# Kernel tuning notes

Hardware: AMD Instinct MI355X
Metric: run time of the kernel (lower is better)

Reference implementation:

```python
import math
import jax, jax.numpy as jnp
import numpy as np

FACTOR = 1  # self.factor
B, L, H, E = 16, 2048, 8, 64


def setup_inputs() -> dict:
    key = jax.random.key(0)
    kq, kk, kv = jax.random.split(key, 3)
    queries = jax.random.normal(kq, (B, L, H, E), dtype=jnp.float32)
    keys = jax.random.normal(kk, (B, L, H, E), dtype=jnp.float32)
    values = jax.random.normal(kv, (B, L, H, E), dtype=jnp.float32)
    return {"queries": queries, "keys": keys, "values": values}


def reference(queries, keys, values):
    # AutoCorrelation forward, agg_mode='speed', inference path (train=False),
    # norm=False, Q == K == V lengths so the pad/truncate branch is a no-op.
    Bb, Ll, Hh, Ee = queries.shape
    # Permute to [B, H, E, L] as the torch code does before FFT / aggregation.
    qp = jnp.transpose(queries, (0, 2, 3, 1))
    kp = jnp.transpose(keys, (0, 2, 3, 1))
    vp = jnp.transpose(values, (0, 2, 3, 1))
    # (1) period-based dependency discovery: circular cross-correlation via FFT
    q_fft = jnp.fft.rfft(qp, axis=-1)
    k_fft = jnp.fft.rfft(kp, axis=-1)
    corr = jnp.fft.irfft(q_fft * jnp.conj(k_fft), n=Ll, axis=-1)  # [B,H,E,L]
    # (2) time delay aggregation (speed mode, inference):
    k = int(FACTOR * math.log(Ll))
    mean_r_qk = jnp.mean(corr, axis=(1, 2))  # mean over head then channel -> [B,L]
    r_qk_top, tao = jax.lax.top_k(mean_r_qk, k)  # [B,k]
    weights = jax.nn.softmax(r_qk_top, axis=-1)  # [B,k]
    # gather into values repeated twice along L  <=>  circular roll by tao
    idx = (jnp.arange(Ll)[None, None, :] + tao[:, :, None]) % Ll  # [B,k,L]
    # [B,1,H,E,L] gathered with [B,k,1,1,L] -> [B,k,H,E,L]
    gathered = jnp.take_along_axis(vp[:, None], idx[:, :, None, None, :], axis=-1)
    agg = jnp.einsum('bk,bkhel->bhel', weights, gathered)  # softmax-weighted sum
    # back to [B, L, H, E]
    return jnp.transpose(agg, (0, 3, 1, 2))
```

## Files before the change

kernel.cpp:

```cpp
#include <hip/hip_runtime.h>
#include <math.h>

#define LN      2048
#define LOG2L   11
#define BB      16
#define HE      512
#define KTOP    7
#define TWO_PI  6.283185307179586f
#define RC      0.70710678118654752f

#define SIG(e)  ((e) ^ (((e) >> 5) & 31))

struct c32 { float x, y; };
__device__ __forceinline__ c32 cmul(c32 a, c32 b) {
    return { a.x * b.x - a.y * b.y, a.x * b.y + a.y * b.x };
}
__device__ __forceinline__ c32 cadd(c32 a, c32 b) { return { a.x + b.x, a.y + b.y }; }
__device__ __forceinline__ c32 csub(c32 a, c32 b) { return { a.x - b.x, a.y - b.y }; }

__device__ __forceinline__ void dft4(c32 a, c32 b, c32 c, c32 d,
                                     c32& y0, c32& y1, c32& y2, c32& y3) {
    c32 t0 = cadd(a, c), t1 = csub(a, c);
    c32 t2 = cadd(b, d);
    c32 t3 = { b.y - d.y, d.x - b.x };
    y0 = cadd(t0, t2);
    y1 = cadd(t1, t3);
    y2 = csub(t0, t2);
    y3 = csub(t1, t3);
}

__device__ __forceinline__ void dft8(const c32* x, c32* y) {
    c32 e0, e1, e2, e3, o0, o1, o2, o3;
    dft4(x[0], x[2], x[4], x[6], e0, e1, e2, e3);
    dft4(x[1], x[3], x[5], x[7], o0, o1, o2, o3);
    c32 p1 = { RC * (o1.x + o1.y), RC * (o1.y - o1.x) };
    c32 p2 = { o2.y, -o2.x };
    c32 p3 = { RC * (o3.y - o3.x), -RC * (o3.x + o3.y) };
    y[0] = cadd(e0, o0); y[4] = csub(e0, o0);
    y[1] = cadd(e1, p1); y[5] = csub(e1, p1);
    y[2] = cadd(e2, p2); y[6] = csub(e2, p2);
    y[3] = cadd(e3, p3); y[7] = csub(e3, p3);
}

__device__ __forceinline__ void mk_tw(int pm, c32* W) {
    float sn, cs;
    __sincosf(-(TWO_PI / (float)LN) * (float)pm, &sn, &cs);
    const c32 w1 = { cs, sn };
    const c32 w2 = cmul(w1, w1);
    const c32 w3 = cmul(w1, w2);
    const c32 w4 = cmul(w2, w2);
    W[0] = w1; W[1] = w2; W[2] = w3; W[3] = w4;
    W[4] = cmul(w1, w4); W[5] = cmul(w2, w4); W[6] = cmul(w3, w4);
}

template<int LOG2M>
__device__ __forceinline__ void r8_ld(float2* Z, int tid, const c32* TW) {
    c32 v[8];
    #pragma unroll
    for (int r = 0; r < 8; ++r) {
        float2 z = Z[SIG(tid + (r << 8))];
        v[r] = { z.x, z.y };
    }
    c32 y[8];
    dft8(v, y);
    #pragma unroll
    for (int kk = 1; kk < 8; ++kk) y[kk] = cmul(y[kk], TW[kk - 1]);
    __syncthreads();
    const int q_ = tid & ((1 << LOG2M) - 1);
    const int ob = q_ + ((tid - q_) << 3);
    #pragma unroll
    for (int kk = 0; kk < 8; ++kk)
        Z[SIG(ob + (kk << LOG2M))] = make_float2(y[kk].x, y[kk].y);
    __syncthreads();
}

__device__ __forceinline__ void r4_final_wg(float2* Z, int tid) {
    c32 v[2][4];
    #pragma unroll
    for (int u = 0; u < 2; ++u) {
        const int j = tid + (u << 8);
        #pragma unroll
        for (int r = 0; r < 4; ++r) {
            float2 z = Z[SIG(j + (r << 9))];
            v[u][r] = { z.x, z.y };
        }
    }
    __syncthreads();
    #pragma unroll
    for (int u = 0; u < 2; ++u) {
        const int j = tid + (u << 8);
        c32 y0, y1, y2, y3;
        dft4(v[u][0], v[u][1], v[u][2], v[u][3], y0, y1, y2, y3);
        Z[SIG(j)]        = make_float2(y0.x, y0.y);
        Z[SIG(j + 512)]  = make_float2(y1.x, y1.y);
        Z[SIG(j + 1024)] = make_float2(y2.x, y2.y);
        Z[SIG(j + 1536)] = make_float2(y3.x, y3.y);
    }
    __syncthreads();
}

__global__ __launch_bounds__(256) void transpose_pack_kernel(
    const float* __restrict__ q, const float* __restrict__ k,
    float* __restrict__ qT, float* __restrict__ kT) {
    __shared__ float2 tile[64][65];
    const int tid = threadIdx.x;
    const int bid = blockIdx.x;
    const int b  = bid >> 8;
    const int lt = (bid >> 3) & 31;
    const int ct = bid & 7;
    const int l0 = lt << 6, c0 = ct << 6;
    const int g16 = tid >> 4;
    const int m16 = (tid & 15) << 2;
    #pragma unroll
    for (int ii = 0; ii < 4; ++ii) {
        const int r = g16 + (ii << 4);
        const size_t src = ((size_t)(b * LN + l0 + r)) * HE + c0 + m16;
        const float4 qv = *(const float4*)(q + src);
        const float4 kv = *(const float4*)(k + src);
        tile[r][m16 + 0] = make_float2(qv.x, kv.x);
        tile[r][m16 + 1] = make_float2(qv.y, kv.y);
        tile[r][m16 + 2] = make_float2(qv.z, kv.z);
        tile[r][m16 + 3] = make_float2(qv.w, kv.w);
    }
    __syncthreads();
    #pragma unroll
    for (int ii = 0; ii < 4; ++ii) {
        const int rc = g16 + (ii << 4);
        const float2 t0 = tile[m16 + 0][rc];
        const float2 t1 = tile[m16 + 1][rc];
        const float2 t2 = tile[m16 + 2][rc];
        const float2 t3 = tile[m16 + 3][rc];
        const size_t dst = ((size_t)(b * HE + c0 + rc)) * LN + l0 + m16;
        *(float4*)(qT + dst) = make_float4(t0.x, t1.x, t2.x, t3.x);
        *(float4*)(kT + dst) = make_float4(t0.y, t1.y, t2.y, t3.y);
    }
}

__global__ __launch_bounds__(256) void fft_reg0_kernel(
    const float* __restrict__ qT, const float* __restrict__ kT,
    float* __restrict__ spec ) {
    __shared__ float2 Z[LN];
    const int tid = threadIdx.x;
    const int wg  = blockIdx.x;
    const int b   = wg >> 7;
    const int c0  = (wg & 127) << 2;

    c32 TW0[7], TW1[7], TW2[7];
    mk_tw(tid, TW0);
    mk_tw(tid & ~7, TW1);
    mk_tw(tid & ~63, TW2);

    float accx[4], accy[4];
    #pragma unroll
    for (int i = 0; i < 4; ++i) { accx[i] = 0.f; accy[i] = 0.f; }
    float a1024 = 0.f;

    const size_t base0 = ((size_t)(b * HE + c0)) << LOG2L;
    c32 v[8];
    #pragma unroll
    for (int r = 0; r < 8; ++r) {
        v[r].x = qT[base0 + tid + (r << 8)];
        v[r].y = kT[base0 + tid + (r << 8)];
    }

    #pragma unroll 1
    for (int ch = 0; ch < 4; ++ch) {
        c32 y[8];
        dft8(v, y);
        #pragma unroll
        for (int kk = 1; kk < 8; ++kk) y[kk] = cmul(y[kk], TW0[kk - 1]);
        __syncthreads();
        #pragma unroll
        for (int kk = 0; kk < 8; ++kk)
            Z[SIG((tid << 3) + kk)] = make_float2(y[kk].x, y[kk].y);
        __syncthreads();

        if (ch < 3) {
            const size_t basen = base0 + ((size_t)(ch + 1) << LOG2L);
            #pragma unroll
            for (int r = 0; r < 8; ++r) {
                v[r].x = qT[basen + tid + (r << 8)];
                v[r].y = kT[basen + tid + (r << 8)];
            }
        }

        r8_ld<3>(Z, tid, TW1);
        r8_ld<6>(Z, tid, TW2);
        r4_final_wg(Z, tid);

        #pragma unroll
        for (int i = 0; i < 4; ++i) {
            const int f = tid + (i << 8);
            const int g = (LN - f) & (LN - 1);
            const float2 zf = Z[SIG(f)];
            const float2 zm = Z[SIG(g)];
            const float Qr = 0.5f * (zf.x + zm.x);
            const float Qi = 0.5f * (zf.y - zm.y);
            const float Kr = 0.5f * (zf.y + zm.y);
            const float Ki = -0.5f * (zf.x - zm.x);
            accx[i] += Qr * Kr + Qi * Ki;
            accy[i] += Qi * Kr - Qr * Ki;
        }
        if (tid == 0) {
            const float2 zf = Z[SIG(1024)];
            a1024 += zf.x * zf.y;
        }
    }
    #pragma unroll
    for (int i = 0; i < 4; ++i) {
        const int f = tid + (i << 8);
        atomicAdd(&spec[((size_t)b * LN + f) * 2 + 0], accx[i]);
        atomicAdd(&spec[((size_t)b * LN + f) * 2 + 1], accy[i]);
    }
    if (tid == 0)
        atomicAdd(&spec[((size_t)b * LN + 1024) * 2 + 0], a1024);
}

template<int LOG2M>
__device__ __forceinline__ void r8_stage(float2* Z, int lane) {
    c32 v[32];
    #pragma unroll
    for (int u = 0; u < 4; ++u) {
        const int j = lane + (u << 6);
        #pragma unroll
        for (int r = 0; r < 8; ++r) {
            float2 z = Z[SIG(j + (r << 8))];
            v[(u << 3) + r] = { z.x, z.y };
        }
    }
    c32 y[32];
    #pragma unroll
    for (int u = 0; u < 4; ++u) {
        const int j  = lane + (u << 6);
        const int pm = j & ~((1 << LOG2M) - 1);
        dft8(&v[u << 3], &y[u << 3]);
        float sn, cs;
        __sincosf(-(TWO_PI / (float)LN) * (float)pm, &sn, &cs);
        c32 base = { cs, sn };
        c32 t = base;
        #pragma unroll
        for (int kk = 1; kk < 8; ++kk) {
            y[(u << 3) + kk] = cmul(y[(u << 3) + kk], t);
            if (kk < 7) t = cmul(t, base);
        }
    }
    __syncthreads();
    #pragma unroll
    for (int u = 0; u < 4; ++u) {
        const int j  = lane + (u << 6);
        const int q_ = j & ((1 << LOG2M) - 1);
        const int ob = q_ + ((j - q_) << 3);
        #pragma unroll
        for (int kk = 0; kk < 8; ++kk) {
            c32 yy = y[(u << 3) + kk];
            Z[SIG(ob + (kk << LOG2M))] = make_float2(yy.x, yy.y);
        }
    }
    __syncthreads();
}

__device__ __forceinline__ void r4_final(float2* Z, int lane) {
    c32 v[32];
    #pragma unroll
    for (int u = 0; u < 8; ++u) {
        const int j = lane + (u << 6);
        #pragma unroll
        for (int r = 0; r < 4; ++r) {
            float2 z = Z[SIG(j + (r << 9))];
            v[(u << 2) + r] = { z.x, z.y };
        }
    }
    __syncthreads();
    #pragma unroll
    for (int u = 0; u < 8; ++u) {
        const int j = lane + (u << 6);
        c32 y0, y1, y2, y3;
        dft4(v[u << 2], v[(u << 2) + 1], v[(u << 2) + 2], v[(u << 2) + 3],
             y0, y1, y2, y3);
        Z[SIG(j)]        = make_float2(y0.x, y0.y);
        Z[SIG(j + 512)]  = make_float2(y1.x, y1.y);
        Z[SIG(j + 1024)] = make_float2(y2.x, y2.y);
        Z[SIG(j + 1536)] = make_float2(y3.x, y3.y);
    }
    __syncthreads();
}

__global__ __launch_bounds__(256) void fft_fused_kernel(
    const float* __restrict__ qg, const float* __restrict__ kg,
    float* __restrict__ spec) {
    __shared__ float2 zb[4][LN];
    const int t    = threadIdx.x;
    const int bid  = blockIdx.x;
    const int wgid = ((bid & 7) << 8) | (bid >> 3);
    const int b    = wgid >> 7;
    const int c0   = (wgid & 127) << 2;
    #pragma unroll
    for (int i = 0; i < 8; ++i) {
        const int l = t + (i << 8);
        const size_t base = (size_t)(b * LN + l) * HE + c0;
        const float4 qv = *(const float4*)(qg + base);
        const float4 kv = *(const float4*)(kg + base);
        const int sl = SIG(l);
        zb[0][sl] = make_float2(qv.x, kv.x);
        zb[1][sl] = make_float2(qv.y, kv.y);
        zb[2][sl] = make_float2(qv.z, kv.z);
        zb[3][sl] = make_float2(qv.w, kv.w);
    }
    __syncthreads();
    const int w    = t >> 6;
    const int lane = t & 63;
    float2* Z = zb[w];
    r8_stage<0>(Z, lane);
    r8_stage<3>(Z, lane);
    r8_stage<6>(Z, lane);
    r4_final(Z, lane);
    float sx[32], sy[32];
    #pragma unroll
    for (int i = 0; i < 32; ++i) {
        const int f = lane + (i << 6);
        const float2 zf = Z[SIG(f)];
        const float2 zm = Z[SIG((LN - f) & (LN - 1))];
        const float Qr = 0.5f * (zf.x + zm.x);
        const float Qi = 0.5f * (zf.y - zm.y);
        const float Kr = 0.5f * (zf.y + zm.y);
        const float Ki = -0.5f * (zf.x - zm.x);
        sx[i] = Qr * Kr + Qi * Ki;
        sy[i] = Qi * Kr - Qr * Ki;
    }
    __syncthreads();
    #pragma unroll
    for (int i = 0; i < 32; ++i) {
        const int f = lane + (i << 6);
        Z[SIG(f)] = make_float2(sx[i], sy[i]);
    }
    __syncthreads();
    #pragma unroll
    for (int i = 0; i < 8; ++i) {
        const int f  = t + (i << 8);
        if (f <= 1024) {
            const int sf = SIG(f);
            const float rx = zb[0][sf].x + zb[1][sf].x + zb[2][sf].x + zb[3][sf].x;
            const float ry = zb[0][sf].y + zb[1][sf].y + zb[2][sf].y + zb[3][sf].y;
            atomicAdd(&spec[((size_t)b * LN + f) * 2 + 0], rx);
            atomicAdd(&spec[((size_t)b * LN + f) * 2 + 1], ry);
        }
    }
}

__device__ __forceinline__ unsigned bitrev11(unsigned x) {
    return __brev(x) >> (32 - LOG2L);
}

__global__ __launch_bounds__(256) void icorr_topk_kernel(
    const float* __restrict__ spec, float* __restrict__ wts, int* __restrict__ tao) {
    __shared__ float2 zbuf[LN];
    __shared__ float2 tw[LN / 2];
    __shared__ float  cr[LN];
    __shared__ float  rv[256];
    __shared__ int    ri[256];
    __shared__ float  topv[KTOP];
    __shared__ int    topi[KTOP];
    const int tid = threadIdx.x;
    const int b   = blockIdx.x;
    for (int p = tid; p < LN / 2; p += 256) {
        float s, c;
        sincosf(-TWO_PI * (float)p / (float)LN, &s, &c);
        tw[p] = make_float2(c, s);
    }
    for (int f = tid; f < LN; f += 256) {
        const int  fs  = (f <= 1024) ? f : (LN - f);
        const float sg = (f <= 1024) ? -1.f : 1.f;
        float sr = spec[((size_t)b * LN + fs) * 2 + 0];
        float si = spec[((size_t)b * LN + fs) * 2 + 1];
        zbuf[bitrev11((unsigned)f)] = make_float2(sr, sg * si);
    }
    __syncthreads();
    for (int s = 0; s < LOG2L; ++s) {
        const int half = 1 << s;
        for (int j = tid; j < LN / 2; j += 256) {
            const int grp = j >> s;
            const int pos = j & (half - 1);
            const int i0  = (grp << (s + 1)) + pos;
            const int i1  = i0 + half;
            const float2 w = tw[pos << (LOG2L - 1 - s)];
            float2 a  = zbuf[i0];
            float2 bv = zbuf[i1];
            float tr = w.x * bv.x - w.y * bv.y;
            float ti = w.x * bv.y + w.y * bv.x;
            zbuf[i0] = make_float2(a.x + tr, a.y + ti);
            zbuf[i1] = make_float2(a.x - tr, a.y - ti);
        }
        __syncthreads();
    }
    const float scale = 1.0f / ((float)LN * (float)HE);
    for (int t = tid; t < LN; t += 256) cr[t] = zbuf[t].x * scale;
    __syncthreads();
    for (int it = 0; it < KTOP; ++it) {
        float mv = -INFINITY;
        int   mi = 0;
        for (int t = tid; t < LN; t += 256) {
            float v = cr[t];
            if (v > mv) { mv = v; mi = t; }
        }
        rv[tid] = mv; ri[tid] = mi;
        __syncthreads();
        for (int off = 128; off > 0; off >>= 1) {
            if (tid < off) {
                float ov = rv[tid + off]; int oi = ri[tid + off];
                if (ov > rv[tid] || (ov == rv[tid] && oi < ri[tid])) {
                    rv[tid] = ov; ri[tid] = oi;
                }
            }
            __syncthreads();
        }
        if (tid == 0) {
            topv[it] = rv[0];
            topi[it] = ri[0];
            cr[ri[0]] = -INFINITY;
        }
        __syncthreads();
    }
    if (tid == 0) {
        float m = topv[0];
        float s = 0.f;
        float ex[KTOP];
        for (int j = 0; j < KTOP; ++j) { ex[j] = __expf(topv[j] - m); s += ex[j]; }
        float inv = 1.0f / s;
        for (int j = 0; j < KTOP; ++j) {
            wts[b * 8 + j] = ex[j] * inv;
            tao[b * 8 + j] = topi[j];
        }
    }
}

__global__ __launch_bounds__(256) void gather_kernel(
    const float* __restrict__ v, const float* __restrict__ wts,
    const int* __restrict__ tao, float* __restrict__ out) {
    __shared__ float lw[KTOP];
    __shared__ int   lt[KTOP];
    const int tid = threadIdx.x;
    const int bid = blockIdx.x;
    const int wg  = ((bid & 7) << 11) | (bid >> 3);
    const long long idx = (long long)wg * 256 + tid;
    const int c4 = (int)(idx & 127);
    const int l  = (int)((idx >> 7) & (LN - 1));
    const int b  = (int)(idx >> 18);
    if (tid < KTOP) {
        lw[tid] = wts[b * 8 + tid];
        lt[tid] = tao[b * 8 + tid];
    }
    __syncthreads();
    const float4* v4 = (const float4*)v;
    float4 a = make_float4(0.f, 0.f, 0.f, 0.f);
    #pragma unroll
    for (int j = 0; j < KTOP; ++j) {
        int ls = (l + lt[j]) & (LN - 1);
        float4 x = v4[((size_t)b * LN + ls) * 128 + c4];
        float w = lw[j];
        a.x += w * x.x; a.y += w * x.y; a.z += w * x.z; a.w += w * x.w;
    }
    ((float4*)out)[idx] = a;
}

extern "C" void kernel_launch(void* const* d_in, const int* in_sizes, int n_in,
                              void* d_out, int out_size, void* d_ws, size_t ws_size,
                              hipStream_t stream) {
    const float* q = (const float*)d_in[0];
    const float* k = (const float*)d_in[1];
    const float* v = (const float*)d_in[2];
    float* out = (float*)d_out;

    const size_t nT   = (size_t)BB * HE * LN;
    const size_t need = nT * 4 + (size_t)BB * LN * 2 * 4 + (size_t)BB * 8 * 8;

    if (ws_size >= need) {
        float* kT   = (float*)d_ws;
        float* spec = kT + nT;
        float* wts  = spec + (size_t)BB * LN * 2;
        int*   tao  = (int*)(wts + BB * 8);
        float* qT   = out;

        hipMemsetAsync(spec, 0, (size_t)BB * LN * 2 * sizeof(float), stream);
        transpose_pack_kernel<<<BB * 32 * 8, 256, 0, stream>>>(q, k, qT, kT);
        fft_reg0_kernel<<<BB * (HE / 4), 256, 0, stream>>>(qT, kT, spec);
        icorr_topk_kernel<<<BB, 256, 0, stream>>>(spec, wts, tao);
        const int n4 = BB * LN * HE / 4;
        gather_kernel<<<n4 / 256, 256, 0, stream>>>(v, wts, tao, out);
    } else {
        float* spec = (float*)d_ws;
        float* wts  = spec + (size_t)BB * LN * 2;
        int*   tao  = (int*)(wts + BB * 8);
        hipMemsetAsync(spec, 0, (size_t)BB * LN * 2 * sizeof(float), stream);
        fft_fused_kernel<<<BB * (HE / 4), 256, 0, stream>>>(q, k, spec);
        icorr_topk_kernel<<<BB, 256, 0, stream>>>(spec, wts, tao);
        const int n4 = BB * LN * HE / 4;
        gather_kernel<<<n4 / 256, 256, 0, stream>>>(v, wts, tao, out);
    }
}
```

Measured before the change: 173.4 us.

## Trim FFT kernel register use: recompute twiddles, drop prefetch, halve channels per block

The FFT kernel no longer keeps three precomputed twiddle arrays and a prefetched next-channel register buffer alive across the loop. Twiddles are recomputed with sincos inside each radix-8 stage, and each block now handles 2 channels instead of 4, which doubles the grid. Launch bounds request 8 blocks per CU. The aim is lower VGPR pressure and higher occupancy. The cost is extra sincos work, the loss of load/compute overlap within a block, and twice as many atomic or partial spectrum accumulations.

```diff
diff --git a/kernel.cpp b/kernel.cpp
--- a/kernel.cpp
+++ b/kernel.cpp
@@ -54,7 +54,7 @@
 }
 
 template<int LOG2M>
-__device__ __forceinline__ void r8_ld(float2* Z, int tid, const c32* TW) {
+__device__ __forceinline__ void r8_ld_t(float2* Z, int tid) {
     c32 v[8];
     #pragma unroll
     for (int r = 0; r < 8; ++r) {
@@ -63,8 +63,10 @@
     }
     c32 y[8];
     dft8(v, y);
-    #pragma unroll
-    for (int kk = 1; kk < 8; ++kk) y[kk] = cmul(y[kk], TW[kk - 1]);
+    c32 W[7];
+    mk_tw(tid & ~((1 << LOG2M) - 1), W);
+    #pragma unroll
+    for (int kk = 1; kk < 8; ++kk) y[kk] = cmul(y[kk], W[kk - 1]);
     __syncthreads();
     const int q_ = tid & ((1 << LOG2M) - 1);
     const int ob = q_ + ((tid - q_) << 3);
@@ -136,19 +138,14 @@
     }
 }
 
-__global__ __launch_bounds__(256) void fft_reg0_kernel(
+__global__ __launch_bounds__(256, 8) void fft_lean_kernel(
     const float* __restrict__ qT, const float* __restrict__ kT,
     float* __restrict__ spec ) {
     __shared__ float2 Z[LN];
     const int tid = threadIdx.x;
     const int wg  = blockIdx.x;
-    const int b   = wg >> 7;
-    const int c0  = (wg & 127) << 2;
-
-    c32 TW0[7], TW1[7], TW2[7];
-    mk_tw(tid, TW0);
-    mk_tw(tid & ~7, TW1);
-    mk_tw(tid & ~63, TW2);
+    const int b   = wg >> 8;
+    const int c0  = (wg & 255) << 1;
 
     float accx[4], accy[4];
     #pragma unroll
@@ -156,36 +153,32 @@
     float a1024 = 0.f;
 
     const size_t base0 = ((size_t)(b * HE + c0)) << LOG2L;
-    c32 v[8];
-    #pragma unroll
-    for (int r = 0; r < 8; ++r) {
-        v[r].x = qT[base0 + tid + (r << 8)];
-        v[r].y = kT[base0 + tid + (r << 8)];
-    }
 
     #pragma unroll 1
-    for (int ch = 0; ch < 4; ++ch) {
+    for (int ch = 0; ch < 2; ++ch) {
+        const size_t base = base0 + ((size_t)ch << LOG2L);
+        c32 v[8];
+        #pragma unroll
+        for (int r = 0; r < 8; ++r) {
+            v[r].x = qT[base + tid + (r << 8)];
+            v[r].y = kT[base + tid + (r << 8)];
+        }
         c32 y[8];
         dft8(v, y);
-        #pragma unroll
-        for (int kk = 1; kk < 8; ++kk) y[kk] = cmul(y[kk], TW0[kk - 1]);
+        {
+            c32 W[7];
+            mk_tw(tid, W);
+            #pragma unroll
+            for (int kk = 1; kk < 8; ++kk) y[kk] = cmul(y[kk], W[kk - 1]);
+        }
         __syncthreads();
         #pragma unroll
         for (int kk = 0; kk < 8; ++kk)
             Z[SIG((tid << 3) + kk)] = make_float2(y[kk].x, y[kk].y);
         __syncthreads();
 
-        if (ch < 3) {
-            const size_t basen = base0 + ((size_t)(ch + 1) << LOG2L);
-            #pragma unroll
-            for (int r = 0; r < 8; ++r) {
-                v[r].x = qT[basen + tid + (r << 8)];
-                v[r].y = kT[basen + tid + (r << 8)];
-            }
-        }
-
-        r8_ld<3>(Z, tid, TW1);
-        r8_ld<6>(Z, tid, TW2);
+        r8_ld_t<3>(Z, tid);
+        r8_ld_t<6>(Z, tid);
         r4_final_wg(Z, tid);
 
         #pragma unroll
@@ -482,7 +475,7 @@
 
         hipMemsetAsync(spec, 0, (size_t)BB * LN * 2 * sizeof(float), stream);
         transpose_pack_kernel<<<BB * 32 * 8, 256, 0, stream>>>(q, k, qT, kT);
-        fft_reg0_kernel<<<BB * (HE / 4), 256, 0, stream>>>(qT, kT, spec);
+        fft_lean_kernel<<<BB * (HE / 2), 256, 0, stream>>>(qT, kT, spec);
         icorr_topk_kernel<<<BB, 256, 0, stream>>>(spec, wts, tao);
         const int n4 = BB * LN * HE / 4;
         gather_kernel<<<n4 / 256, 256, 0, stream>>>(v, wts, tao, out);
```

New measurement: 404.9 us. 2.33x slower.
